# Kernel tuning notes

Hardware: AMD Instinct MI355X
Metric: run time of the kernel (lower is better)

## Reference

```python
import jax, jax.numpy as jnp
import numpy as np

B, S, D = 2, 2048, 2048
NH, NKV, DH = 16, 4, 128
NG = NH // NKV  # query heads per kv head


def rope_apply(x, cos, sin):
    # x: [B, H, S, DH]; cos/sin: [S, DH//2]
    x1, x2 = jnp.split(x, 2, axis=-1)
    c = cos[None, None, :, :]
    s = sin[None, None, :, :]
    return jnp.concatenate([x1 * c - x2 * s, x1 * s + x2 * c], axis=-1)


def setup_inputs() -> dict:
    key = jax.random.key(0)
    ks = jax.random.split(key, 6)
    x = jax.random.normal(ks[0], (B, S, D), dtype=jnp.float32)
    # real RoPE frequencies
    inv_freq = 1.0 / (10000.0 ** (jnp.arange(0, DH // 2, dtype=jnp.float32) * 2.0 / DH))
    angles = jnp.arange(S, dtype=jnp.float32)[:, None] * inv_freq[None, :]  # [S, DH//2]
    cos, sin = jnp.cos(angles), jnp.sin(angles)
    mask = jnp.tril(jnp.ones((S, S), dtype=bool))[None, None]  # causal [1,1,S,S]
    sc = 0.02
    Wq = jax.random.normal(ks[1], (D, NH * DH), dtype=jnp.float32) * sc
    Wk = jax.random.normal(ks[2], (D, NKV * DH), dtype=jnp.float32) * sc
    Wv = jax.random.normal(ks[3], (D, NKV * DH), dtype=jnp.float32) * sc
    Wo = jax.random.normal(ks[4], (NH * DH, D), dtype=jnp.float32) * sc
    return {"x": x, "cos": cos, "sin": sin, "mask": mask,
            "Wq": Wq, "Wk": Wk, "Wv": Wv, "Wo": Wo}


def reference(x, cos, sin, mask, Wq, Wk, Wv, Wo):
    b, s, _ = x.shape
    q = (x @ Wq).reshape(b, s, NH, DH).transpose(0, 2, 1, 3)    # [B,NH,S,DH]
    k = (x @ Wk).reshape(b, s, NKV, DH).transpose(0, 2, 1, 3)   # [B,NKV,S,DH]
    v = (x @ Wv).reshape(b, s, NKV, DH).transpose(0, 2, 1, 3)
    q = rope_apply(q, cos, sin)
    k = rope_apply(k, cos, sin)
    new_kv_cache = (k, v)
    k_exp = jnp.repeat(k, NG, axis=1)  # [B,NH,S,DH]
    v_exp = jnp.repeat(v, NG, axis=1)
    scale = jnp.float32(np.sqrt(DH))
    scores = jnp.einsum('bhqd,bhkd->bhqk', q, k_exp) / scale
    scores = jnp.where(mask, scores, jnp.float32(-1e9))
    weights = jax.nn.softmax(scores, axis=-1)
    context = jnp.einsum('bhqk,bhkd->bhqd', weights, v_exp)
    context = context.transpose(0, 2, 1, 3).reshape(b, s, NH * DH)
    output = context @ Wo
    return output, new_kv_cache[0], new_kv_cache[1]
```

## Files before the change

### kernel.cpp

```cpp
#include <hip/hip_runtime.h>
#include <stdint.h>

#define Bb 2
#define Ss 2048
#define Dd 2048
#define NHh 16
#define NKVv 4
#define DHh 128
#define Mm_ (Bb*Ss)
#define NQq (NHh*DHh)

using bf16x8 = __attribute__((ext_vector_type(8))) __bf16;
using f32x4  = __attribute__((ext_vector_type(4))) float;

__device__ __forceinline__ unsigned short f2bf(float f) {
  unsigned u = __float_as_uint(f);
  u += 0x7fffu + ((u >> 16) & 1u);
  return (unsigned short)(u >> 16);
}
__device__ __forceinline__ float bf2f(unsigned short s) {
  return __uint_as_float(((unsigned)s) << 16);
}

__global__ void k_convert(const float* __restrict__ in, unsigned short* __restrict__ out, int n4) {
  const int i = blockIdx.x * blockDim.x + threadIdx.x;
  if (i >= n4) return;
  const float4 v = ((const float4*)in)[i];
  ushort4 o;
  o.x = f2bf(v.x); o.y = f2bf(v.y); o.z = f2bf(v.z); o.w = f2bf(v.w);
  ((ushort4*)out)[i] = o;
}

__global__ __launch_bounds__(256) void k_transpose_all(
    const float* __restrict__ Wq, const float* __restrict__ Wk,
    const float* __restrict__ Wv, const float* __restrict__ Wo,
    unsigned short* __restrict__ wqkvT, unsigned short* __restrict__ woT) {
  __shared__ float tile[32][33];
  int bid = blockIdx.x;
  const float* in;
  unsigned short* out;
  int Nn;
  if (bid < 4096)      { in = Wq; out = wqkvT;                        Nn = 2048; }
  else if (bid < 5120) { in = Wk; out = wqkvT + (size_t)2048 * 2048;  Nn = 512;  bid -= 4096; }
  else if (bid < 6144) { in = Wv; out = wqkvT + (size_t)2560 * 2048;  Nn = 512;  bid -= 5120; }
  else                 { in = Wo; out = woT;                          Nn = 2048; bid -= 6144; }
  const int nbx = Nn >> 5;
  const int n0 = (bid % nbx) * 32, k0 = (bid / nbx) * 32;
  const int tx = threadIdx.x & 31, ty = threadIdx.x >> 5;
  #pragma unroll
  for (int i = 0; i < 4; ++i)
    tile[ty + i * 8][tx] = in[(size_t)(k0 + ty + i * 8) * Nn + n0 + tx];
  __syncthreads();
  #pragma unroll
  for (int i = 0; i < 4; ++i)
    out[(size_t)(n0 + ty + i * 8) * 2048 + k0 + tx] = f2bf(tile[tx][ty + i * 8]);
}

template<int BNW, int MODE>
__global__ __launch_bounds__(512) void k_gemm256(const unsigned short* __restrict__ A,
                                                 const unsigned short* __restrict__ BT,
                                                 int Kdim,
                                                 unsigned short* __restrict__ Qo,
                                                 float* __restrict__ kfo,
                                                 float* __restrict__ outV,
                                                 unsigned short* __restrict__ vTb,
                                                 float* __restrict__ Cf) {
  __shared__ unsigned short ldsA[2][16384];
  __shared__ unsigned short ldsB[2][4096 * BNW];
  const int tid = threadIdx.x;
  const int lane = tid & 63;
  const int lg = lane >> 4, ll = lane & 15;
  const int wid = tid >> 6;
  const int wm = wid >> 2, wn = wid & 3;
  const int m0 = blockIdx.y << 8;
  const int n0 = blockIdx.x * (64 * BNW);

  f32x4 acc[8][BNW] = {};
  bf16x8 bfr[BNW];

  auto stage_A = [&](int buf, int kt, int s) {
    const int c = (s << 9) + tid;
    const int row = c >> 3, c16 = c & 7;
    const int csrc = (c16 ^ (row & 7)) << 3;
    const unsigned short* src = A + (size_t)(m0 + row) * Kdim + kt * 64 + csrc;
    __builtin_amdgcn_global_load_lds(
        (const __attribute__((address_space(1))) void*)src,
        (__attribute__((address_space(3))) void*)(&ldsA[buf][0] + c * 8), 16, 0, 0);
  };
  auto stage_B = [&](int buf, int kt, int s) {
    const int c = (s << 9) + tid;
    const int row = c >> 3, c16 = c & 7;
    const int csrc = (c16 ^ (row & 7)) << 3;
    const unsigned short* src = BT + (size_t)(n0 + row) * Kdim + kt * 64 + csrc;
    __builtin_amdgcn_global_load_lds(
        (const __attribute__((address_space(1))) void*)src,
        (__attribute__((address_space(3))) void*)(&ldsB[buf][0] + c * 8), 16, 0, 0);
  };

  #pragma unroll
  for (int s = 0; s < 4; ++s) stage_A(0, 0, s);
  #pragma unroll
  for (int s = 0; s < BNW; ++s) stage_B(0, 0, s);
  __syncthreads();

  const int nkt = Kdim >> 6;
  int cur = 0;
  for (int kt = 0; kt < nkt; ++kt) {
    const int nxt = cur ^ 1;
    const bool hn = (kt + 1 < nkt);
    const char* Atl = (const char*)&ldsA[cur][0];
    const char* Btl = (const char*)&ldsB[cur][0];

    auto rdB = [&](int ks) {
      #pragma unroll
      for (int i = 0; i < BNW; ++i) {
        const int r = wn * (16 * BNW) + i * 16 + ll;
        bfr[i] = *(const bf16x8*)(const void*)(
            Btl + r * 128 + ((ks * 64 + lg * 16) ^ ((r & 7) << 4)));
      }
    };
    auto quad = [&](int mh, int ks) {
      bf16x8 af[4];
      #pragma unroll
      for (int i = 0; i < 4; ++i) {
        const int r = wm * 128 + (mh * 4 + i) * 16 + ll;
        af[i] = *(const bf16x8*)(const void*)(
            Atl + r * 128 + ((ks * 64 + lg * 16) ^ ((r & 7) << 4)));
      }
      __builtin_amdgcn_s_setprio(1);
      #pragma unroll
      for (int i = 0; i < 4; ++i)
        #pragma unroll
        for (int n = 0; n < BNW; ++n)
          acc[mh * 4 + i][n] =
              __builtin_amdgcn_mfma_f32_16x16x32_bf16(af[i], bfr[n], acc[mh * 4 + i][n], 0, 0, 0);
      __builtin_amdgcn_s_setprio(0);
    };

    rdB(0);
    if (hn) { stage_A(nxt, kt + 1, 0); stage_A(nxt, kt + 1, 1);
              stage_A(nxt, kt + 1, 2); stage_A(nxt, kt + 1, 3); }
    __builtin_amdgcn_s_barrier();
    quad(0, 0);
    __builtin_amdgcn_s_barrier();
    if (hn) {
      #pragma unroll
      for (int s = 0; s < BNW; ++s) stage_B(nxt, kt + 1, s);
    }
    __builtin_amdgcn_s_barrier();
    quad(1, 0);
    __builtin_amdgcn_s_barrier();
    rdB(1);
    __builtin_amdgcn_s_barrier();
    quad(0, 1);
    __builtin_amdgcn_s_barrier();
    quad(1, 1);
    if (hn) {
      asm volatile("s_waitcnt vmcnt(0)" ::: "memory");
    }
    __builtin_amdgcn_s_barrier();
    cur ^= 1;
  }

  #pragma unroll
  for (int mi = 0; mi < 8; ++mi)
    #pragma unroll
    for (int ni = 0; ni < BNW; ++ni) {
      const int row4 = m0 + wm * 128 + mi * 16 + lg * 4;
      const int col = n0 + wn * (16 * BNW) + ni * 16 + ll;
      if (MODE == 1) {
        #pragma unroll
        for (int jj = 0; jj < 4; ++jj)
          Cf[(size_t)(row4 + jj) * 2048 + col] = acc[mi][ni][jj];
      } else {
        if (col < 2048) {
          #pragma unroll
          for (int jj = 0; jj < 4; ++jj)
            Qo[(size_t)(row4 + jj) * 2048 + col] = f2bf(acc[mi][ni][jj]);
        } else if (col < 2560) {
          #pragma unroll
          for (int jj = 0; jj < 4; ++jj)
            kfo[(size_t)(row4 + jj) * 512 + (col - 2048)] = acc[mi][ni][jj];
        } else {
          const int kv = (col - 2560) >> 7, dh = (col - 2560) & 127;
          const int b = row4 >> 11, s0 = row4 & 2047;
          #pragma unroll
          for (int jj = 0; jj < 4; ++jj)
            outV[((size_t)(b * NKVv + kv) * Ss + s0 + jj) * DHh + dh] = acc[mi][ni][jj];
          ushort4 pk;
          pk.x = f2bf(acc[mi][ni][0]); pk.y = f2bf(acc[mi][ni][1]);
          pk.z = f2bf(acc[mi][ni][2]); pk.w = f2bf(acc[mi][ni][3]);
          *(ushort4*)&vTb[((size_t)(b * NKVv + kv) * DHh + dh) * Ss + s0] = pk;
        }
      }
    }
}

__global__ void k_rope_k(const float* __restrict__ kf, const float* __restrict__ cosT,
                         const float* __restrict__ sinT, float* __restrict__ outK,
                         unsigned short* __restrict__ kbb) {
  const int idx = blockIdx.x * blockDim.x + threadIdx.x;
  if (idx >= Mm_ * NKVv * 64) return;
  const int dh2 = idx & 63;
  const int kv = (idx >> 6) & 3;
  const int m = idx >> 8;
  const int s = m & (Ss - 1);
  const int b = m >> 11;
  const size_t src = (size_t)m * 512 + kv * DHh + dh2;
  const float x1 = kf[src], x2 = kf[src + 64];
  const float c = cosT[s * 64 + dh2], sn = sinT[s * 64 + dh2];
  const float o1 = x1 * c - x2 * sn, o2 = x1 * sn + x2 * c;
  const size_t dst = ((size_t)(b * NKVv + kv) * Ss + s) * DHh + dh2;
  outK[dst] = o1; outK[dst + 64] = o2;
  kbb[dst] = f2bf(o1); kbb[dst + 64] = f2bf(o2);
}

__global__ __launch_bounds__(256) void k_attn(const unsigned short* __restrict__ qb,
                                              const unsigned short* __restrict__ kb,
                                              const unsigned short* __restrict__ vT,
                                              const float* __restrict__ cosT,
                                              const float* __restrict__ sinT,
                                              unsigned short* __restrict__ ctxb) {
  const int linear = blockIdx.y * 32 + blockIdx.x;
  const int r = linear >> 8;
  const int u = linear & 255;
  const int q2 = u & 7;
  const int bh = u >> 3;
  int qt;
  if      (r == 0) qt = q2;
  else if (r == 1) qt = 15 - q2;
  else if (r == 2) qt = 16 + q2;
  else             qt = 31 - q2;

  const int b = bh >> 4, h = bh & 15;
  const int kvh = h >> 2;
  const int tid = threadIdx.x, wid = tid >> 6, lane = tid & 63;
  const int lg = lane >> 4, ll = lane & 15;
  __shared__ unsigned short kts[8192];
  __shared__ unsigned short vts[8192];
  __shared__ unsigned short p_s[4096];
  const char* ktc = (const char*)kts;
  const char* vtc = (const char*)vts;
  char* pwc = (char*)p_s + wid * 2048;
  const int swz = (ll & 7) << 4;
  const unsigned short* kbase = kb + (size_t)(b * NKVv + kvh) * Ss * DHh;
  const unsigned short* vbase = vT + (size_t)(b * NKVv + kvh) * DHh * Ss;
  const int qrow_f = qt * 64 + wid * 16 + ll;
  const unsigned short* qrow = qb + (size_t)(b * Ss + qrow_f) * NQq + h * DHh;

  uint4 rq[4];
  #pragma unroll
  for (int ks = 0; ks < 4; ++ks)
    rq[ks] = *(const uint4*)(const void*)(qrow + ks * 32 + lg * 8);
  bf16x8 qfr[4];
  {
    const unsigned short* rqs = (const unsigned short*)rq;
    unsigned short qtmp[4][8];
    const float scq = 0.12751746595544662f;
    #pragma unroll
    for (int ksh = 0; ksh < 2; ++ksh) {
      #pragma unroll
      for (int e = 0; e < 8; ++e) {
        const int dh2 = ksh * 32 + lg * 8 + e;
        const float c = cosT[qrow_f * 64 + dh2], sn = sinT[qrow_f * 64 + dh2];
        const float x1 = bf2f(rqs[ksh * 8 + e]);
        const float x2 = bf2f(rqs[(ksh + 2) * 8 + e]);
        qtmp[ksh][e]     = f2bf((x1 * c - x2 * sn) * scq);
        qtmp[ksh + 2][e] = f2bf((x1 * sn + x2 * c) * scq);
      }
    }
    #pragma unroll
    for (int ks = 0; ks < 4; ++ks) qfr[ks] = *(const bf16x8*)(const void*)qtmp[ks];
  }

  union { unsigned int u4[4]; bf16x8 v; } onesu;
  onesu.u4[0] = onesu.u4[1] = onesu.u4[2] = onesu.u4[3] = 0x3F803F80u;
  const bf16x8 onesf = onesu.v;

  f32x4 ctx[9] = {};
  const int qr0 = qt * 64 + wid * 16 + lg * 4;
  const int nkt = qt + 1;

  auto stage_k = [&](int ktile) {
    #pragma unroll
    for (int i = 0; i < 4; ++i) {
      const int s = i * 256 + tid;
      const int krow = s >> 4, kcs = (s & 15) ^ (krow & 7);
      const unsigned short* ksrc = kbase + (size_t)(ktile * 64 + krow) * DHh + kcs * 8;
      __builtin_amdgcn_global_load_lds(
          (const __attribute__((address_space(1))) void*)ksrc,
          (__attribute__((address_space(3))) void*)(kts + (i * 256 + wid * 64) * 8), 16, 0, 0);
    }
  };
  auto stage_v = [&](int ktile) {
    #pragma unroll
    for (int i = 0; i < 4; ++i) {
      const int s = i * 256 + tid;
      const int vrow = s >> 3, vcs = (s & 7) ^ (vrow & 7);
      const unsigned short* vsrc = vbase + (size_t)vrow * Ss + ktile * 64 + vcs * 8;
      __builtin_amdgcn_global_load_lds(
          (const __attribute__((address_space(1))) void*)vsrc,
          (__attribute__((address_space(3))) void*)(vts + (i * 256 + wid * 64) * 8), 16, 0, 0);
    }
  };

  stage_k(0);
  __syncthreads();
  for (int kt = 0; kt < nkt; ++kt) {
    stage_v(kt);
    f32x4 sc[4] = {};
    __builtin_amdgcn_s_setprio(1);
    #pragma unroll
    for (int ks = 0; ks < 4; ++ks) {
      #pragma unroll
      for (int cb = 0; cb < 4; ++cb) {
        const bf16x8 kfr = *(const bf16x8*)(const void*)(
            ktc + ((cb * 16 + ll) << 8) + (((ks << 6) + (lg << 4)) ^ swz));
        sc[cb] = __builtin_amdgcn_mfma_f32_16x16x32_bf16(qfr[ks], kfr, sc[cb], 0, 0, 0);
      }
    }
    __builtin_amdgcn_s_setprio(0);
    const bool domask = (kt == qt);
    float pv[4][4];
    #pragma unroll
    for (int cb = 0; cb < 4; ++cb)
      #pragma unroll
      for (int j = 0; j < 4; ++j) {
        float s = sc[cb][j];
        if (domask && (kt * 64 + cb * 16 + ll > qr0 + j)) s = -1e30f;
        pv[cb][j] = exp2f(s - 8.656170245333781f);
      }
    #pragma unroll
    for (int cb = 0; cb < 4; ++cb)
      #pragma unroll
      for (int j = 0; j < 4; ++j) {
        const int prow = lg * 4 + j;
        *(unsigned short*)(pwc + (prow << 7) + (((cb << 5) + (ll << 1)) ^ ((prow & 7) << 4))) =
            (unsigned short)((__float_as_uint(pv[cb][j]) + 0x8000u) >> 16);
      }
    __syncthreads();
    if (kt + 1 < nkt) stage_k(kt + 1);
    __builtin_amdgcn_s_setprio(1);
    #pragma unroll
    for (int k2 = 0; k2 < 2; ++k2) {
      const bf16x8 pa = *(const bf16x8*)(const void*)(
          pwc + (ll << 7) + (((k2 << 6) + (lg << 4)) ^ swz));
      #pragma unroll
      for (int ob = 0; ob < 8; ++ob) {
        const bf16x8 vfr = *(const bf16x8*)(const void*)(
            vtc + ((ob * 16 + ll) << 7) + (((k2 << 6) + (lg << 4)) ^ swz));
        ctx[ob] = __builtin_amdgcn_mfma_f32_16x16x32_bf16(pa, vfr, ctx[ob], 0, 0, 0);
      }
      ctx[8] = __builtin_amdgcn_mfma_f32_16x16x32_bf16(pa, onesf, ctx[8], 0, 0, 0);
    }
    __builtin_amdgcn_s_setprio(0);
    __syncthreads();
  }
  #pragma unroll
  for (int j = 0; j < 4; ++j) {
    const float inv = 1.f / ctx[8][j];
    unsigned short* crow = ctxb + (size_t)(b * Ss + qr0 + j) * NQq + h * DHh;
    #pragma unroll
    for (int ob = 0; ob < 8; ++ob)
      crow[ob * 16 + ll] = f2bf(ctx[ob][j] * inv);
  }
}

extern "C" void kernel_launch(void* const* d_in, const int* in_sizes, int n_in,
                              void* d_out, int out_size, void* d_ws, size_t ws_size,
                              hipStream_t stream) {
  const float* x    = (const float*)d_in[0];
  const float* cosT = (const float*)d_in[1];
  const float* sinT = (const float*)d_in[2];
  const float* Wq   = (const float*)d_in[4];
  const float* Wk   = (const float*)d_in[5];
  const float* Wv   = (const float*)d_in[6];
  const float* Wo   = (const float*)d_in[7];
  float* out  = (float*)d_out;
  float* outK = out + (size_t)Mm_ * Dd;
  float* outV = outK + (size_t)Bb * NKVv * Ss * DHh;

  char* ws = (char*)d_ws;
  size_t off = 0;
  auto alloc = [&](size_t bytes) -> void* {
    void* p = ws + off;
    off += (bytes + 255) & ~(size_t)255;
    return p;
  };
  unsigned short* xb    = (unsigned short*)alloc((size_t)Mm_ * Dd * 2);
  unsigned short* wqkvT = (unsigned short*)alloc((size_t)3072 * Dd * 2);
  unsigned short* woT   = (unsigned short*)alloc((size_t)Dd * NQq * 2);
  unsigned short* qfb   = (unsigned short*)alloc((size_t)Mm_ * NQq * 2);
  float*          kf    = (float*)alloc((size_t)Mm_ * 512 * 4);
  unsigned short* kbb   = (unsigned short*)alloc((size_t)Bb * NKVv * Ss * DHh * 2);
  unsigned short* vTb   = (unsigned short*)alloc((size_t)Bb * NKVv * Ss * DHh * 2);
  unsigned short* ctxb  = (unsigned short*)alloc((size_t)Mm_ * NQq * 2);
  if (off > ws_size) return;

  k_convert<<<(Mm_ * Dd / 4 + 255) / 256, 256, 0, stream>>>(x, xb, Mm_ * Dd / 4);
  k_transpose_all<<<10240, 256, 0, stream>>>(Wq, Wk, Wv, Wo, wqkvT, woT);
  k_gemm256<3, 0><<<dim3(16, 16), 512, 0, stream>>>(
      xb, wqkvT, Dd, qfb, kf, outV, vTb, (float*)nullptr);
  k_rope_k<<<(Mm_ * NKVv * 64 + 255) / 256, 256, 0, stream>>>(kf, cosT, sinT, outK, kbb);
  k_attn<<<dim3(32, 32), 256, 0, stream>>>(qfb, kbb, vTb, cosT, sinT, ctxb);
  k_gemm256<2, 1><<<dim3(16, 16), 512, 0, stream>>>(
      ctxb, woT, NQq, (unsigned short*)nullptr, (float*)nullptr,
      (float*)nullptr, (unsigned short*)nullptr, out);
}
```

Baseline: 199.6 us.

## Shrink attention tiles to 32x32 with two-wave blocks and rebalanced causal schedule

The attention kernel now uses 32-row query tiles and 32-column key tiles with 128-thread blocks (two waves) instead of 64x64 tiles with four waves. The grid doubles to 2048 blocks, and the causal-tile pairing is reworked so that short and long query tiles interleave. LDS use per block drops and the causal diagonal wastes less work, which is meant to raise occupancy and load balance. In exchange, each block reloads K/V more often relative to its compute and pays more loop and barrier overhead per MFMA.

```diff
diff --git a/kernel.cpp b/kernel.cpp
--- a/kernel.cpp
+++ b/kernel.cpp
@@ -215,37 +215,36 @@
   kbb[dst] = f2bf(o1); kbb[dst + 64] = f2bf(o2);
 }
 
-__global__ __launch_bounds__(256) void k_attn(const unsigned short* __restrict__ qb,
+__global__ __launch_bounds__(128) void k_attn(const unsigned short* __restrict__ qb,
                                               const unsigned short* __restrict__ kb,
                                               const unsigned short* __restrict__ vT,
                                               const float* __restrict__ cosT,
                                               const float* __restrict__ sinT,
                                               unsigned short* __restrict__ ctxb) {
-  const int linear = blockIdx.y * 32 + blockIdx.x;
+  const int linear = blockIdx.y * 64 + blockIdx.x;
   const int r = linear >> 8;
   const int u = linear & 255;
-  const int q2 = u & 7;
+  const int q3 = u & 7;
   const int bh = u >> 3;
-  int qt;
-  if      (r == 0) qt = q2;
-  else if (r == 1) qt = 15 - q2;
-  else if (r == 2) qt = 16 + q2;
-  else             qt = 31 - q2;
+  int qq;
+  if (r & 1) qq = 63 - (((r >> 1) << 3) + q3);
+  else       qq = ((r >> 1) << 3) + q3;
 
   const int b = bh >> 4, h = bh & 15;
   const int kvh = h >> 2;
   const int tid = threadIdx.x, wid = tid >> 6, lane = tid & 63;
   const int lg = lane >> 4, ll = lane & 15;
-  __shared__ unsigned short kts[8192];
-  __shared__ unsigned short vts[8192];
-  __shared__ unsigned short p_s[4096];
+  __shared__ unsigned short kts[32 * 128];
+  __shared__ unsigned short vts[128 * 32];
+  __shared__ unsigned short p_s[1024];
   const char* ktc = (const char*)kts;
   const char* vtc = (const char*)vts;
-  char* pwc = (char*)p_s + wid * 2048;
-  const int swz = (ll & 7) << 4;
+  char* pwc = (char*)p_s + wid * 1024;
+  const int swzk = (ll & 7) << 4;
+  const int swz4 = (ll & 3) << 4;
   const unsigned short* kbase = kb + (size_t)(b * NKVv + kvh) * Ss * DHh;
   const unsigned short* vbase = vT + (size_t)(b * NKVv + kvh) * DHh * Ss;
-  const int qrow_f = qt * 64 + wid * 16 + ll;
+  const int qrow_f = qq * 32 + wid * 16 + ll;
   const unsigned short* qrow = qb + (size_t)(b * Ss + qrow_f) * NQq + h * DHh;
 
   uint4 rq[4];
@@ -278,29 +277,31 @@
   const bf16x8 onesf = onesu.v;
 
   f32x4 ctx[9] = {};
-  const int qr0 = qt * 64 + wid * 16 + lg * 4;
-  const int nkt = qt + 1;
+  const int qr0 = qq * 32 + wid * 16 + lg * 4;
+  const int nkt = qq + 1;
 
   auto stage_k = [&](int ktile) {
     #pragma unroll
     for (int i = 0; i < 4; ++i) {
-      const int s = i * 256 + tid;
-      const int krow = s >> 4, kcs = (s & 15) ^ (krow & 7);
-      const unsigned short* ksrc = kbase + (size_t)(ktile * 64 + krow) * DHh + kcs * 8;
+      const int c = i * 128 + tid;
+      const int krow = c >> 4, kc = c & 15;
+      const int kcs = (kc ^ (krow & 7)) << 3;
+      const unsigned short* ksrc = kbase + (size_t)(ktile * 32 + krow) * DHh + kcs;
       __builtin_amdgcn_global_load_lds(
           (const __attribute__((address_space(1))) void*)ksrc,
-          (__attribute__((address_space(3))) void*)(kts + (i * 256 + wid * 64) * 8), 16, 0, 0);
+          (__attribute__((address_space(3))) void*)(kts + (i * 128 + wid * 64) * 8), 16, 0, 0);
     }
   };
   auto stage_v = [&](int ktile) {
     #pragma unroll
     for (int i = 0; i < 4; ++i) {
-      const int s = i * 256 + tid;
-      const int vrow = s >> 3, vcs = (s & 7) ^ (vrow & 7);
-      const unsigned short* vsrc = vbase + (size_t)vrow * Ss + ktile * 64 + vcs * 8;
+      const int c = i * 128 + tid;
+      const int vrow = c >> 2, vc = c & 3;
+      const int vcs = (vc ^ (vrow & 3)) << 3;
+      const unsigned short* vsrc = vbase + (size_t)vrow * Ss + ktile * 32 + vcs;
       __builtin_amdgcn_global_load_lds(
           (const __attribute__((address_space(1))) void*)vsrc,
-          (__attribute__((address_space(3))) void*)(vts + (i * 256 + wid * 64) * 8), 16, 0, 0);
+          (__attribute__((address_space(3))) void*)(vts + (i * 128 + wid * 64) * 8), 16, 0, 0);
     }
   };
 
@@ -308,47 +309,46 @@
   __syncthreads();
   for (int kt = 0; kt < nkt; ++kt) {
     stage_v(kt);
-    f32x4 sc[4] = {};
+    f32x4 sc[2] = {};
     __builtin_amdgcn_s_setprio(1);
     #pragma unroll
     for (int ks = 0; ks < 4; ++ks) {
       #pragma unroll
-      for (int cb = 0; cb < 4; ++cb) {
+      for (int cb = 0; cb < 2; ++cb) {
         const bf16x8 kfr = *(const bf16x8*)(const void*)(
-            ktc + ((cb * 16 + ll) << 8) + (((ks << 6) + (lg << 4)) ^ swz));
+            ktc + ((cb * 16 + ll) << 8) + (((ks << 6) + (lg << 4)) ^ swzk));
         sc[cb] = __builtin_amdgcn_mfma_f32_16x16x32_bf16(qfr[ks], kfr, sc[cb], 0, 0, 0);
       }
     }
     __builtin_amdgcn_s_setprio(0);
-    const bool domask = (kt == qt);
-    float pv[4][4];
-    #pragma unroll
-    for (int cb = 0; cb < 4; ++cb)
+    const bool domask = (kt == qq);
+    float pv[2][4];
+    #pragma unroll
+    for (int cb = 0; cb < 2; ++cb)
       #pragma unroll
       for (int j = 0; j < 4; ++j) {
         float s = sc[cb][j];
-        if (domask && (kt * 64 + cb * 16 + ll > qr0 + j)) s = -1e30f;
+        if (domask && (kt * 32 + cb * 16 + ll > qr0 + j)) s = -1e30f;
         pv[cb][j] = exp2f(s - 8.656170245333781f);
       }
     #pragma unroll
-    for (int cb = 0; cb < 4; ++cb)
+    for (int cb = 0; cb < 2; ++cb)
       #pragma unroll
       for (int j = 0; j < 4; ++j) {
         const int prow = lg * 4 + j;
-        *(unsigned short*)(pwc + (prow << 7) + (((cb << 5) + (ll << 1)) ^ ((prow & 7) << 4))) =
+        *(unsigned short*)(pwc + (prow << 6) + (((cb << 5) + (ll << 1)) ^ ((prow & 3) << 4))) =
             (unsigned short)((__float_as_uint(pv[cb][j]) + 0x8000u) >> 16);
       }
     __syncthreads();
     if (kt + 1 < nkt) stage_k(kt + 1);
     __builtin_amdgcn_s_setprio(1);
-    #pragma unroll
-    for (int k2 = 0; k2 < 2; ++k2) {
+    {
       const bf16x8 pa = *(const bf16x8*)(const void*)(
-          pwc + (ll << 7) + (((k2 << 6) + (lg << 4)) ^ swz));
+          pwc + (ll << 6) + ((lg << 4) ^ swz4));
       #pragma unroll
       for (int ob = 0; ob < 8; ++ob) {
         const bf16x8 vfr = *(const bf16x8*)(const void*)(
-            vtc + ((ob * 16 + ll) << 7) + (((k2 << 6) + (lg << 4)) ^ swz));
+            vtc + ((ob * 16 + ll) << 6) + ((lg << 4) ^ swz4));
         ctx[ob] = __builtin_amdgcn_mfma_f32_16x16x32_bf16(pa, vfr, ctx[ob], 0, 0, 0);
       }
       ctx[8] = __builtin_amdgcn_mfma_f32_16x16x32_bf16(pa, onesf, ctx[8], 0, 0, 0);
@@ -402,7 +402,7 @@
   k_gemm256<3, 0><<<dim3(16, 16), 512, 0, stream>>>(
       xb, wqkvT, Dd, qfb, kf, outV, vTb, (float*)nullptr);
   k_rope_k<<<(Mm_ * NKVv * 64 + 255) / 256, 256, 0, stream>>>(kf, cosT, sinT, outK, kbb);
-  k_attn<<<dim3(32, 32), 256, 0, stream>>>(qfb, kbb, vTb, cosT, sinT, ctxb);
+  k_attn<<<dim3(64, 32), 128, 0, stream>>>(qfb, kbb, vTb, cosT, sinT, ctxb);
   k_gemm256<2, 1><<<dim3(16, 16), 512, 0, stream>>>(
       ctxb, woT, NQq, (unsigned short*)nullptr, (float*)nullptr,
       (float*)nullptr, (unsigned short*)nullptr, out);
```

New measurement: 199.3 us. No clear change (-0.1%).
